# Kernel optimization log

Hardware: AMD Instinct MI355X
Metric: run time of the kernel (lower is better)

Reference implementation:

```python
import jax, jax.numpy as jnp
import numpy as np

N = 50000   # nodes
E = 800000  # edges
D = 96      # feature dim


def setup_inputs() -> dict:
    key = jax.random.key(0)
    k1, k2, k3, k4 = jax.random.split(key, 4)
    scale = 1.0 / np.sqrt(D)
    return {
        "x": jax.random.normal(k1, (N, D), dtype=jnp.float32),
        "edge_index": jax.random.randint(k2, (2, E), 0, N, dtype=jnp.int64),
        "W1": jax.random.normal(k3, (D, D), dtype=jnp.float32) * scale,
        "b1": jnp.zeros((D,), dtype=jnp.float32),
        "W2": jax.random.normal(k4, (D, D), dtype=jnp.float32) * scale,
        "b2": jnp.zeros((D,), dtype=jnp.float32),
    }


def _gcn_conv(x, src, dst, W, b, n_nodes):
    # PyG GCNConv: linear transform, add self-loops, symmetric normalization,
    # scatter-add aggregation from src (row) to dst (col), then bias.
    h = x @ W  # [N, D_out]
    loops = jnp.arange(n_nodes, dtype=src.dtype)
    s = jnp.concatenate([src, loops])  # [E+N]
    d = jnp.concatenate([dst, loops])  # [E+N]
    deg = jax.ops.segment_sum(jnp.ones_like(d, dtype=h.dtype), d, num_segments=n_nodes)
    dinv = jnp.where(deg > 0, jax.lax.rsqrt(deg), 0.0)  # deg^-1/2, 0 for isolated
    norm = dinv[s] * dinv[d]  # [E+N]
    msg = norm[:, None] * h[s]  # gather + scale
    out = jax.ops.segment_sum(msg, d, num_segments=n_nodes)  # scatter-add
    return out + b


def reference(x, edge_index, W1, b1, W2, b2):
    src, dst = edge_index[0], edge_index[1]
    # dropout p=0.0 -> identity. ReLU after every layer (loop break never fires).
    h = _gcn_conv(x, src, dst, W1, b1, N)
    h = jax.nn.relu(h)
    h = _gcn_conv(h, src, dst, W2, b2, N)
    h = jax.nn.relu(h)
    return h
```

## Files before the change

kernel.cpp:

```cpp
#include <hip/hip_runtime.h>
#include <hip/hip_fp16.h>

#define NN 50000
#define EE 800000
#define DD 96

#define NBIN 196
#define CE   4096
#define CB   196
#define EPT2 16



__global__ __launch_bounds__(256) void k_hist(const int* __restrict__ ei,
                                              int* __restrict__ histB) {
    __shared__ int hist[NBIN];
    int t = threadIdx.x;
    if (t < NBIN) hist[t] = 0;
    __syncthreads();
    int e0 = blockIdx.x * CE;
#pragma unroll
    for (int k = 0; k < EPT2; ++k) {
        int e = e0 + k * 256 + t;
        if (e < EE) atomicAdd(&hist[ei[EE + e] >> 8], 1);
    }
    __syncthreads();
    if (t < NBIN) histB[t * CB + blockIdx.x] = hist[t];
}


__global__ __launch_bounds__(256) void k_scan_bins(int* __restrict__ histB,
                                                   int* __restrict__ binTot) {
    __shared__ int sh[256];
    int t = threadIdx.x;
    int b = blockIdx.x;
    int v = (t < CB) ? histB[b * CB + t] : 0;
    sh[t] = v;
    __syncthreads();
    for (int off = 1; off < 256; off <<= 1) {
        int u = (t >= off) ? sh[t - off] : 0;
        __syncthreads();
        sh[t] += u;
        __syncthreads();
    }
    if (t < CB) histB[b * CB + t] = sh[t] - v;
    if (t == 255) binTot[b] = sh[255];
}


__global__ __launch_bounds__(256) void k_scan_tot(const int* __restrict__ binTot,
                                                  int* __restrict__ binbase) {
    __shared__ int sh[256];
    int t = threadIdx.x;
    int v = (t < NBIN) ? binTot[t] : 0;
    sh[t] = v;
    __syncthreads();
    for (int off = 1; off < 256; off <<= 1) {
        int u = (t >= off) ? sh[t - off] : 0;
        __syncthreads();
        sh[t] += u;
        __syncthreads();
    }
    if (t < NBIN) binbase[t] = sh[t] - v;
    if (t == 0) binbase[NBIN] = EE;
}


__global__ __launch_bounds__(256) void k_scatter_bins(const int* __restrict__ ei,
                                                      const int* __restrict__ histB,
                                                      const int* __restrict__ binbase,
                                                      int* __restrict__ packed) {
    __shared__ int hist[NBIN];
    __shared__ int lofs[NBIN + 1];
    __shared__ int cur[NBIN];
    __shared__ int sstart[NBIN];
    __shared__ int buf[CE];
    __shared__ int sh[256];
    int t = threadIdx.x;
    int e0 = blockIdx.x * CE;
    int nE = min(CE, EE - e0);

    int s[EPT2], d[EPT2];
#pragma unroll
    for (int k = 0; k < EPT2; ++k) {
        int e = e0 + k * 256 + t;
        s[k] = (e < EE) ? ei[e] : 0;
        d[k] = (e < EE) ? ei[EE + e] : -1;
    }
    if (t < NBIN) hist[t] = 0;
    __syncthreads();
#pragma unroll
    for (int k = 0; k < EPT2; ++k)
        if (d[k] >= 0) atomicAdd(&hist[d[k] >> 8], 1);
    __syncthreads();
    int v = (t < NBIN) ? hist[t] : 0;
    sh[t] = v;
    __syncthreads();
    for (int off = 1; off < 256; off <<= 1) {
        int u = (t >= off) ? sh[t - off] : 0;
        __syncthreads();
        sh[t] += u;
        __syncthreads();
    }
    if (t < NBIN) { lofs[t] = sh[t] - v; cur[t] = sh[t] - v; }
    if (t == 0) lofs[NBIN] = nE;
    if (t < NBIN) sstart[t] = binbase[t] + histB[t * CB + blockIdx.x];
    __syncthreads();
#pragma unroll
    for (int k = 0; k < EPT2; ++k)
        if (d[k] >= 0) {
            int b = d[k] >> 8;
            int pos = atomicAdd(&cur[b], 1);
            buf[pos] = s[k] | ((d[k] & 0xFF) << 16);
        }
    __syncthreads();
    for (int i = t; i < nE; i += 256) {
        int blo = 0, bhi = NBIN;
        while (bhi - blo > 1) {
            int mid = (blo + bhi) >> 1;
            if (lofs[mid] <= i) blo = mid; else bhi = mid;
        }
        packed[sstart[blo] + (i - lofs[blo])] = buf[i];
    }
}


__global__ __launch_bounds__(256) void k_csr(const int* __restrict__ packed,
                                             const int* __restrict__ binbase,
                                             int* __restrict__ rp,
                                             float* __restrict__ dinv,
                                             int* __restrict__ col,
                                             const float* __restrict__ x,
                                             __half* __restrict__ xh) {
    __shared__ int h256[256];
    __shared__ int cur[256];
    __shared__ int sh[256];
    __shared__ float sdinv[256];
    int t = threadIdx.x;
    int b = blockIdx.x;
    int base = binbase[b];
    int nE = binbase[b + 1] - base;

    h256[t] = 0;
    __syncthreads();
    for (int i = t; i < nE; i += 256)
        atomicAdd(&h256[(packed[base + i] >> 16) & 0xFF], 1);
    __syncthreads();
    int v = h256[t];
    sh[t] = v;
    __syncthreads();
    for (int off = 1; off < 256; off <<= 1) {
        int u = (t >= off) ? sh[t - off] : 0;
        __syncthreads();
        sh[t] += u;
        __syncthreads();
    }
    int ex = sh[t] - v;
    cur[t] = ex;
    float di = rsqrtf((float)(v + 1));
    sdinv[t] = di;
    int node = b * 256 + t;
    if (node <= NN) rp[node] = base + ex;
    if (node < NN) dinv[node] = di;
    __syncthreads();
    for (int i = t; i < nE; i += 256) {
        int pv = packed[base + i];
        int pos = atomicAdd(&cur[(pv >> 16) & 0xFF], 1);
        col[base + pos] = pv & 0xFFFF;
    }
    for (int i = t; i < 256 * 12; i += 256) {
        int rr = i / 12;
        int cc = i % 12;
        int r = b * 256 + rr;
        if (r < NN) {
            float sc = sdinv[rr];
            const float4* xx = (const float4*)x + (size_t)r * 24 + cc * 2;
            float4 f0 = xx[0], f1 = xx[1];
            __half h[8];
            h[0] = __float2half_rn(sc * f0.x); h[1] = __float2half_rn(sc * f0.y);
            h[2] = __float2half_rn(sc * f0.z); h[3] = __float2half_rn(sc * f0.w);
            h[4] = __float2half_rn(sc * f1.x); h[5] = __float2half_rn(sc * f1.y);
            h[6] = __float2half_rn(sc * f1.z); h[7] = __float2half_rn(sc * f1.w);
            ((uint4*)xh)[(size_t)r * 12 + cc] = *(uint4*)h;
        }
    }
}


template <int FINAL>
__global__ __launch_bounds__(384) void k_fused(const __half* __restrict__ xh,
                                               const int* __restrict__ rp,
                                               const int* __restrict__ col,
                                               const float* __restrict__ dinv,
                                               const float* __restrict__ W,
                                               const float* __restrict__ b,
                                               __half* __restrict__ acth,
                                               float* __restrict__ outf) {
    __shared__ __half Wl[DD * DD];
    __shared__ __half Al[32][104];
    int t = threadIdx.x;
    for (int i = t; i < DD * DD / 8; i += 384) {
        const float4* ww = (const float4*)W;
        float4 f0 = ww[i * 2], f1 = ww[i * 2 + 1];
        __half h[8];
        h[0] = __float2half_rn(f0.x); h[1] = __float2half_rn(f0.y);
        h[2] = __float2half_rn(f0.z); h[3] = __float2half_rn(f0.w);
        h[4] = __float2half_rn(f1.x); h[5] = __float2half_rn(f1.y);
        h[6] = __float2half_rn(f1.z); h[7] = __float2half_rn(f1.w);
        ((uint4*)Wl)[i] = *(uint4*)h;
    }

    int c  = t % 12;
    int ny = t / 12;
    int d = blockIdx.x * 32 + ny;
    const uint4* h4 = (const uint4*)xh;

    if (d < NN) {
        union U { uint4 u; __half2 h[4]; };
        float2 aA[4] = {{0,0},{0,0},{0,0},{0,0}};
        float2 aB[4] = {{0,0},{0,0},{0,0},{0,0}};
        int j0 = rp[d], j1 = rp[d + 1];
        int j = j0;
        for (; j + 3 < j1; j += 4) {
            int s0 = col[j], s1 = col[j+1], s2 = col[j+2], s3 = col[j+3];
            U v0, v1, v2, v3;
            v0.u = h4[s0 * 12 + c];
            v1.u = h4[s1 * 12 + c];
            v2.u = h4[s2 * 12 + c];
            v3.u = h4[s3 * 12 + c];
#pragma unroll
            for (int k = 0; k < 4; ++k) {
                float2 f0 = __half22float2(v0.h[k]);
                float2 f1 = __half22float2(v1.h[k]);
                float2 f2 = __half22float2(v2.h[k]);
                float2 f3 = __half22float2(v3.h[k]);
                aA[k].x += f0.x + f1.x; aA[k].y += f0.y + f1.y;
                aB[k].x += f2.x + f3.x; aB[k].y += f2.y + f3.y;
            }
        }
        for (; j < j1; ++j) {
            U v; v.u = h4[col[j] * 12 + c];
#pragma unroll
            for (int k = 0; k < 4; ++k) {
                float2 f = __half22float2(v.h[k]);
                aA[k].x += f.x; aA[k].y += f.y;
            }
        }
        U self; self.u = h4[d * 12 + c];
        float dd = dinv[d];
        __half hv[8];
#pragma unroll
        for (int k = 0; k < 4; ++k) {
            float2 fs = __half22float2(self.h[k]);
            hv[2*k]   = __float2half_rn(dd * (aA[k].x + aB[k].x + fs.x));
            hv[2*k+1] = __float2half_rn(dd * (aA[k].y + aB[k].y + fs.y));
        }
        *(uint4*)&Al[ny][c * 8] = *(uint4*)hv;
    }
    __syncthreads();

    int tx = t % 24;
    int ry = t / 24;
    int c0 = tx * 4;
    float a0x = 0.f, a0y = 0.f, a0z = 0.f, a0w = 0.f;
    float a1x = 0.f, a1y = 0.f, a1z = 0.f, a1w = 0.f;
#pragma unroll 4
    for (int k = 0; k < DD; k += 2) {
        uint2 wv0 = *(const uint2*)&Wl[k * DD + c0];
        uint2 wv1 = *(const uint2*)&Wl[(k + 1) * DD + c0];
        const __half2* wh0 = (const __half2*)&wv0;
        const __half2* wh1 = (const __half2*)&wv1;
        float2 w0a = __half22float2(wh0[0]);
        float2 w0b = __half22float2(wh0[1]);
        float2 w1a = __half22float2(wh1[0]);
        float2 w1b = __half22float2(wh1[1]);
        float2 ra = __half22float2(*(const __half2*)&Al[ry][k]);
        float2 rb = __half22float2(*(const __half2*)&Al[ry + 16][k]);
        a0x += ra.x * w0a.x + ra.y * w1a.x;
        a0y += ra.x * w0a.y + ra.y * w1a.y;
        a0z += ra.x * w0b.x + ra.y * w1b.x;
        a0w += ra.x * w0b.y + ra.y * w1b.y;
        a1x += rb.x * w0a.x + rb.y * w1a.x;
        a1y += rb.x * w0a.y + rb.y * w1a.y;
        a1z += rb.x * w0b.x + rb.y * w1b.x;
        a1w += rb.x * w0b.y + rb.y * w1b.y;
    }
    float4 bb = *(const float4*)&b[c0];
    int g0 = blockIdx.x * 32 + ry;
    int g1 = g0 + 16;
    float r0x = fmaxf(a0x + bb.x, 0.f), r0y = fmaxf(a0y + bb.y, 0.f);
    float r0z = fmaxf(a0z + bb.z, 0.f), r0w = fmaxf(a0w + bb.w, 0.f);
    float r1x = fmaxf(a1x + bb.x, 0.f), r1y = fmaxf(a1y + bb.y, 0.f);
    float r1z = fmaxf(a1z + bb.z, 0.f), r1w = fmaxf(a1w + bb.w, 0.f);
    if (g0 < NN) {
        if (FINAL) {
            *(float4*)&outf[g0 * DD + c0] = make_float4(r0x, r0y, r0z, r0w);
        } else {
            float sc = dinv[g0];
            __half h[4];
            h[0] = __float2half_rn(sc * r0x); h[1] = __float2half_rn(sc * r0y);
            h[2] = __float2half_rn(sc * r0z); h[3] = __float2half_rn(sc * r0w);
            *(uint2*)&acth[g0 * DD + c0] = *(uint2*)h;
        }
    }
    if (g1 < NN) {
        if (FINAL) {
            *(float4*)&outf[g1 * DD + c0] = make_float4(r1x, r1y, r1z, r1w);
        } else {
            float sc = dinv[g1];
            __half h[4];
            h[0] = __float2half_rn(sc * r1x); h[1] = __float2half_rn(sc * r1y);
            h[2] = __float2half_rn(sc * r1z); h[3] = __float2half_rn(sc * r1w);
            *(uint2*)&acth[g1 * DD + c0] = *(uint2*)h;
        }
    }
}


extern "C" void kernel_launch(void* const* d_in, const int* in_sizes, int n_in,
                              void* d_out, int out_size, void* d_ws, size_t ws_size,
                              hipStream_t stream) {
    const float* x  = (const float*)d_in[0];
    const int*   ei = (const int*)d_in[1];
    const float* W1 = (const float*)d_in[2];
    const float* b1 = (const float*)d_in[3];
    const float* W2 = (const float*)d_in[4];
    const float* b2 = (const float*)d_in[5];
    float* out = (float*)d_out;

    char* p = (char*)d_ws;
    int*   histB   = (int*)p;   p += ((size_t)NBIN * CB * 4 + 255) & ~(size_t)255;
    int*   binTot  = (int*)p;   p += ((size_t)NBIN * 4 + 255) & ~(size_t)255;
    int*   binbase = (int*)p;   p += ((size_t)(NBIN + 1) * 4 + 255) & ~(size_t)255;
    int*   rp      = (int*)p;   p += ((size_t)(NN + 1) * 4 + 255) & ~(size_t)255;
    float* dinv    = (float*)p; p += ((size_t)NN * 4 + 255) & ~(size_t)255;
    int*   col     = (int*)p;   p += ((size_t)EE * 4 + 255) & ~(size_t)255;
    __half* bufA   = (__half*)p; p += ((size_t)NN * DD * 2 + 255) & ~(size_t)255;
    __half* bufB   = (__half*)p;
    int*   packed  = (int*)bufB;

    k_hist<<<CB, 256, 0, stream>>>(ei, histB);
    k_scan_bins<<<NBIN, 256, 0, stream>>>(histB, binTot);
    k_scan_tot<<<1, 256, 0, stream>>>(binTot, binbase);
    k_scatter_bins<<<CB, 256, 0, stream>>>(ei, histB, binbase, packed);
    k_csr<<<NBIN, 256, 0, stream>>>(packed, binbase, rp, dinv, col, x, bufA);

    k_fused<0><<<(NN + 31) / 32, 384, 0, stream>>>(bufA, rp, col, dinv, W1, b1,
                                                   bufB, nullptr);

    k_fused<1><<<(NN + 31) / 32, 384, 0, stream>>>(bufB, rp, col, dinv, W2, b2,
                                                   nullptr, out);
}
```

Baseline: 147.2 us.

## Split each node's neighbor gather across two thread groups, halve nodes per block

Each destination node's edge list is now split between two 12-thread groups that take alternating edges, and the partial sums are combined through shared memory. This doubles the memory-level parallelism per node in the gather. Blocks now cover 16 nodes instead of 32, and the aggregated row is kept in fp32 shared memory, so the dense transform does one row per thread. In exchange the grid doubles, so the W-to-half conversion into LDS is repeated twice as often, and there is an extra barrier plus less reuse of the W tile per block.

```diff
diff --git a/kernel.cpp b/kernel.cpp
--- a/kernel.cpp
+++ b/kernel.cpp
@@ -197,7 +197,7 @@
                                                __half* __restrict__ acth,
                                                float* __restrict__ outf) {
     __shared__ __half Wl[DD * DD];
-    __shared__ __half Al[32][104];
+    __shared__ float Al[16][100];
     int t = threadIdx.x;
     for (int i = t; i < DD * DD / 8; i += 384) {
         const float4* ww = (const float4*)W;
@@ -210,19 +210,21 @@
         ((uint4*)Wl)[i] = *(uint4*)h;
     }
 
-    int c  = t % 12;
-    int ny = t / 12;
-    int d = blockIdx.x * 32 + ny;
+    int lane = t % 24;
+    int c  = lane % 12;
+    int g  = lane / 12;
+    int ny = t / 24;
+    int d = blockIdx.x * 16 + ny;
     const uint4* h4 = (const uint4*)xh;
 
+    union U { uint4 u; __half2 h[4]; };
+    float2 aA[4] = {{0,0},{0,0},{0,0},{0,0}};
+    float2 aB[4] = {{0,0},{0,0},{0,0},{0,0}};
     if (d < NN) {
-        union U { uint4 u; __half2 h[4]; };
-        float2 aA[4] = {{0,0},{0,0},{0,0},{0,0}};
-        float2 aB[4] = {{0,0},{0,0},{0,0},{0,0}};
         int j0 = rp[d], j1 = rp[d + 1];
-        int j = j0;
-        for (; j + 3 < j1; j += 4) {
-            int s0 = col[j], s1 = col[j+1], s2 = col[j+2], s3 = col[j+3];
+        int j = j0 + g;
+        for (; j + 6 < j1; j += 8) {
+            int s0 = col[j], s1 = col[j+2], s2 = col[j+4], s3 = col[j+6];
             U v0, v1, v2, v3;
             v0.u = h4[s0 * 12 + c];
             v1.u = h4[s1 * 12 + c];
@@ -238,7 +240,7 @@
                 aB[k].x += f2.x + f3.x; aB[k].y += f2.y + f3.y;
             }
         }
-        for (; j < j1; ++j) {
+        for (; j < j1; j += 2) {
             U v; v.u = h4[col[j] * 12 + c];
 #pragma unroll
             for (int k = 0; k < 4; ++k) {
@@ -246,16 +248,35 @@
                 aA[k].x += f.x; aA[k].y += f.y;
             }
         }
+    }
+    if (d < NN && g == 1) {
+        *(float4*)&Al[ny][c * 8] =
+            make_float4(aA[0].x + aB[0].x, aA[0].y + aB[0].y,
+                        aA[1].x + aB[1].x, aA[1].y + aB[1].y);
+        *(float4*)&Al[ny][c * 8 + 4] =
+            make_float4(aA[2].x + aB[2].x, aA[2].y + aB[2].y,
+                        aA[3].x + aB[3].x, aA[3].y + aB[3].y);
+    }
+    __syncthreads();
+    if (d < NN && g == 0) {
         U self; self.u = h4[d * 12 + c];
         float dd = dinv[d];
-        __half hv[8];
-#pragma unroll
-        for (int k = 0; k < 4; ++k) {
-            float2 fs = __half22float2(self.h[k]);
-            hv[2*k]   = __float2half_rn(dd * (aA[k].x + aB[k].x + fs.x));
-            hv[2*k+1] = __float2half_rn(dd * (aA[k].y + aB[k].y + fs.y));
-        }
-        *(uint4*)&Al[ny][c * 8] = *(uint4*)hv;
+        float4 q0 = *(float4*)&Al[ny][c * 8];
+        float4 q1 = *(float4*)&Al[ny][c * 8 + 4];
+        float2 fs0 = __half22float2(self.h[0]);
+        float2 fs1 = __half22float2(self.h[1]);
+        float2 fs2 = __half22float2(self.h[2]);
+        float2 fs3 = __half22float2(self.h[3]);
+        *(float4*)&Al[ny][c * 8] = make_float4(
+            dd * (aA[0].x + aB[0].x + q0.x + fs0.x),
+            dd * (aA[0].y + aB[0].y + q0.y + fs0.y),
+            dd * (aA[1].x + aB[1].x + q0.z + fs1.x),
+            dd * (aA[1].y + aB[1].y + q0.w + fs1.y));
+        *(float4*)&Al[ny][c * 8 + 4] = make_float4(
+            dd * (aA[2].x + aB[2].x + q1.x + fs2.x),
+            dd * (aA[2].y + aB[2].y + q1.y + fs2.y),
+            dd * (aA[3].x + aB[3].x + q1.z + fs3.x),
+            dd * (aA[3].y + aB[3].y + q1.w + fs3.y));
     }
     __syncthreads();
 
@@ -263,35 +284,19 @@
     int ry = t / 24;
     int c0 = tx * 4;
     float a0x = 0.f, a0y = 0.f, a0z = 0.f, a0w = 0.f;
-    float a1x = 0.f, a1y = 0.f, a1z = 0.f, a1w = 0.f;
-#pragma unroll 4
-    for (int k = 0; k < DD; k += 2) {
-        uint2 wv0 = *(const uint2*)&Wl[k * DD + c0];
-        uint2 wv1 = *(const uint2*)&Wl[(k + 1) * DD + c0];
-        const __half2* wh0 = (const __half2*)&wv0;
-        const __half2* wh1 = (const __half2*)&wv1;
-        float2 w0a = __half22float2(wh0[0]);
-        float2 w0b = __half22float2(wh0[1]);
-        float2 w1a = __half22float2(wh1[0]);
-        float2 w1b = __half22float2(wh1[1]);
-        float2 ra = __half22float2(*(const __half2*)&Al[ry][k]);
-        float2 rb = __half22float2(*(const __half2*)&Al[ry + 16][k]);
-        a0x += ra.x * w0a.x + ra.y * w1a.x;
-        a0y += ra.x * w0a.y + ra.y * w1a.y;
-        a0z += ra.x * w0b.x + ra.y * w1b.x;
-        a0w += ra.x * w0b.y + ra.y * w1b.y;
-        a1x += rb.x * w0a.x + rb.y * w1a.x;
-        a1y += rb.x * w0a.y + rb.y * w1a.y;
-        a1z += rb.x * w0b.x + rb.y * w1b.x;
-        a1w += rb.x * w0b.y + rb.y * w1b.y;
+#pragma unroll 8
+    for (int k = 0; k < DD; ++k) {
+        uint2 wv = *(const uint2*)&Wl[k * DD + c0];
+        const __half2* wh = (const __half2*)&wv;
+        float2 w01 = __half22float2(wh[0]);
+        float2 w23 = __half22float2(wh[1]);
+        float r0 = Al[ry][k];
+        a0x += r0 * w01.x; a0y += r0 * w01.y; a0z += r0 * w23.x; a0w += r0 * w23.y;
     }
     float4 bb = *(const float4*)&b[c0];
-    int g0 = blockIdx.x * 32 + ry;
-    int g1 = g0 + 16;
+    int g0 = blockIdx.x * 16 + ry;
     float r0x = fmaxf(a0x + bb.x, 0.f), r0y = fmaxf(a0y + bb.y, 0.f);
     float r0z = fmaxf(a0z + bb.z, 0.f), r0w = fmaxf(a0w + bb.w, 0.f);
-    float r1x = fmaxf(a1x + bb.x, 0.f), r1y = fmaxf(a1y + bb.y, 0.f);
-    float r1z = fmaxf(a1z + bb.z, 0.f), r1w = fmaxf(a1w + bb.w, 0.f);
     if (g0 < NN) {
         if (FINAL) {
             *(float4*)&outf[g0 * DD + c0] = make_float4(r0x, r0y, r0z, r0w);
@@ -301,17 +306,6 @@
             h[0] = __float2half_rn(sc * r0x); h[1] = __float2half_rn(sc * r0y);
             h[2] = __float2half_rn(sc * r0z); h[3] = __float2half_rn(sc * r0w);
             *(uint2*)&acth[g0 * DD + c0] = *(uint2*)h;
-        }
-    }
-    if (g1 < NN) {
-        if (FINAL) {
-            *(float4*)&outf[g1 * DD + c0] = make_float4(r1x, r1y, r1z, r1w);
-        } else {
-            float sc = dinv[g1];
-            __half h[4];
-            h[0] = __float2half_rn(sc * r1x); h[1] = __float2half_rn(sc * r1y);
-            h[2] = __float2half_rn(sc * r1z); h[3] = __float2half_rn(sc * r1w);
-            *(uint2*)&acth[g1 * DD + c0] = *(uint2*)h;
         }
     }
 }
@@ -345,9 +339,9 @@
     k_scatter_bins<<<CB, 256, 0, stream>>>(ei, histB, binbase, packed);
     k_csr<<<NBIN, 256, 0, stream>>>(packed, binbase, rp, dinv, col, x, bufA);
 
-    k_fused<0><<<(NN + 31) / 32, 384, 0, stream>>>(bufA, rp, col, dinv, W1, b1,
+    k_fused<0><<<(NN + 15) / 16, 384, 0, stream>>>(bufA, rp, col, dinv, W1, b1,
                                                    bufB, nullptr);
 
-    k_fused<1><<<(NN + 31) / 32, 384, 0, stream>>>(bufB, rp, col, dinv, W2, b2,
+    k_fused<1><<<(NN + 15) / 16, 384, 0, stream>>>(bufB, rp, col, dinv, W2, b2,
                                                    nullptr, out);
 }
```

After: 144.9 us. Within noise of the previous version (-1.6%).
